# Kernel optimization log

Hardware: AMD Instinct MI355X
Metric: run time of the kernel (lower is better)

The kernel has to match this reference:

```python
import jax, jax.numpy as jnp
import numpy as np

B, R, L = 1, 256, 384
IN_DIM, PAIR_DIM, N_HEADS = 128, 128, 8
HEAD_DIM = IN_DIM // N_HEADS
FF_MULT = 4


def layer_norm(x, g, b, eps=1e-5):
    mu = jnp.mean(x, axis=-1, keepdims=True)
    var = jnp.mean((x - mu) ** 2, axis=-1, keepdims=True)
    return (x - mu) * jax.lax.rsqrt(var + eps) * g + b


def setup_inputs() -> dict:
    key = jax.random.key(0)
    ks = jax.random.split(key, 12)
    s = 0.02
    return {
        "x": jax.random.normal(ks[0], (B, L, L, PAIR_DIM), jnp.float32),
        "m": jax.random.normal(ks[1], (B, R, L, IN_DIM), jnp.float32),
        "ln1_g": jnp.ones((PAIR_DIM,), jnp.float32),
        "ln1_b": jnp.zeros((PAIR_DIM,), jnp.float32),
        "ln2_g": jnp.ones((IN_DIM,), jnp.float32),
        "ln2_b": jnp.zeros((IN_DIM,), jnp.float32),
        "ln3_g": jnp.ones((IN_DIM,), jnp.float32),
        "ln3_b": jnp.zeros((IN_DIM,), jnp.float32),
        "w1": jax.random.normal(ks[2], (PAIR_DIM, N_HEADS), jnp.float32) * s,
        "b1": jnp.zeros((N_HEADS,), jnp.float32),
        "w2": jax.random.normal(ks[3], (IN_DIM, HEAD_DIM), jnp.float32) * s,
        "b2": jnp.zeros((HEAD_DIM,), jnp.float32),
        "ffw1": jax.random.normal(ks[4], (IN_DIM, IN_DIM * FF_MULT), jnp.float32) * s,
        "ffb1": jnp.zeros((IN_DIM * FF_MULT,), jnp.float32),
        "ffw2": jax.random.normal(ks[5], (IN_DIM * FF_MULT, IN_DIM), jnp.float32) * s,
        "ffb2": jnp.zeros((IN_DIM,), jnp.float32),
    }


def reference(x, m, ln1_g, ln1_b, ln2_g, ln2_b, ln3_g, ln3_b,
              w1, b1, w2, b2, ffw1, ffb1, ffw2, ffb2):
    # symmetrize pair features: [b, i, j, d]
    pair = (x + jnp.swapaxes(x, 1, 2)) * 0.5
    pair = layer_norm(pair, ln1_g, ln1_b)
    # attention logits per head, softmax over j (axis=-2): [b, i, j, h]
    attn = jax.nn.softmax(pair @ w1 + b1, axis=-2)
    # values: [b, r, j, d_head]
    values = layer_norm(m, ln2_g, ln2_b) @ w2 + b2
    # [b,i,j,h] x [b,r,j,d] -> [b,r,i,h,d]
    attn_out = jnp.einsum('bijh,brjd->brihd', attn, values)
    attn_out = attn_out.reshape(*attn_out.shape[:3], -1)  # [b,r,i,h*d]
    out = m + attn_out
    residue = layer_norm(out, ln3_g, ln3_b)
    ff = jax.nn.relu(residue @ ffw1 + ffb1) @ ffw2 + ffb2  # dropout off (eval)
    return out + ff
```

## Files before the change

kernel.cpp:

```cpp
#include <hip/hip_runtime.h>

typedef __attribute__((ext_vector_type(8))) short bf16x8;
typedef __attribute__((ext_vector_type(4))) float f32x4;

constexpr int L  = 384;
constexpr int R  = 256;
constexpr int D  = 128;
constexpr int NH = 8;
constexpr int HD = 16;
constexpr int FF = 512;

#define MFMA16(a, b, c) __builtin_amdgcn_mfma_f32_16x16x32_bf16((a), (b), (c), 0, 0, 0)

__device__ inline unsigned short f2bf(float f) {
    unsigned u = __builtin_bit_cast(unsigned, f);
    u += 0x7fffu + ((u >> 16) & 1u);
    return (unsigned short)(u >> 16);
}
__device__ inline float bf2f(unsigned short h) {
    unsigned u = ((unsigned)h) << 16;
    return __builtin_bit_cast(float, u);
}

__device__ inline int tri_row(int q) {
    int i = (int)((769.0f - sqrtf((float)(591361 - 8 * q))) * 0.5f);
    while ((i + 1) * (769 - (i + 1)) / 2 <= q) ++i;
    while (i * (769 - i) / 2 > q) --i;
    return i;
}

__global__ void k_prep(const float* __restrict__ w1,
                       const float* __restrict__ w2,
                       const float* __restrict__ ffw1,
                       const float* __restrict__ ffw2,
                       const float* __restrict__ g3,
                       const float* __restrict__ b3,
                       const float* __restrict__ ffb1,
                       unsigned short* __restrict__ w1p,
                       unsigned short* __restrict__ w2p,
                       unsigned short* __restrict__ w1gF,
                       unsigned short* __restrict__ w2tF,
                       float2* __restrict__ c1c2) {
    const int idx = blockIdx.x * 256 + threadIdx.x;
    {
        const int fi = idx >> 9, rem = idx & 511, l = rem >> 3, e = rem & 7;
        const int lr2 = l & 15, lg2 = l >> 4;
        const int n = fi >> 2, ks = fi & 3;
        const int ch = n * 16 + lr2, k = ks * 32 + lg2 * 8 + e;
        w1gF[idx] = f2bf(g3[k] * ffw1[(size_t)k * FF + ch]);
    }
    {
        const int fi = idx >> 9, rem = idx & 511, l = rem >> 3, e = rem & 7;
        const int lr2 = l & 15, lg2 = l >> 4;
        const int n = fi >> 4, Ks = fi & 15;
        const int ch = n * 16 + lr2, k = Ks * 32 + lg2 * 8 + e;
        w2tF[idx] = f2bf(ffw2[(size_t)k * D + ch]);
    }
    if (idx < 16 * D) {
        const int n = idx >> 7, k = idx & 127;
        w1p[idx] = (n < NH) ? f2bf(w1[(size_t)k * NH + n]) : (unsigned short)0;
        w2p[idx] = f2bf(w2[(size_t)k * HD + n]);
    }
    if (blockIdx.x < 2) {
        const int n = blockIdx.x * 256 + threadIdx.x;
        float c1 = 0.f, c2 = 0.f;
        for (int k = 0; k < D; ++k) {
            const float w = ffw1[(size_t)k * FF + n];
            c1 += g3[k] * w;
            c2 += b3[k] * w;
        }
        c1c2[n] = make_float2(c1, c2 + ffb1[n]);
    }
}

__global__ void k_plv(const float* __restrict__ x,
                      const float* __restrict__ g1,
                      const float* __restrict__ bt1,
                      const unsigned short* __restrict__ w1p,
                      const float* __restrict__ b1,
                      float* __restrict__ logits,
                      const float* __restrict__ m_,
                      const float* __restrict__ g2,
                      const float* __restrict__ bt2,
                      const unsigned short* __restrict__ w2p,
                      const float* __restrict__ b2,
                      unsigned short* __restrict__ VtT) {
    __shared__ unsigned short nrm[64][136];
    __shared__ int ij[64];
    const int tid = threadIdx.x;

    if (blockIdx.x < 1155) {
        const int q0 = blockIdx.x * 64;
        {
            const int pr = tid >> 2, part = tid & 3;
            const int q = q0 + pr;
            const int i = tri_row(q);
            const int j = i + (q - i * (769 - i) / 2);
            if (part == 0) ij[pr] = (i << 16) | j;
            const float* xa = x + ((size_t)i * L + j) * D + part * 32;
            const float* xb = x + ((size_t)j * L + i) * D + part * 32;
            float v[32];
            float s = 0.f, sq = 0.f;
            #pragma unroll
            for (int q8 = 0; q8 < 8; ++q8) {
                const float4 a = ((const float4*)xa)[q8];
                const float4 b = ((const float4*)xb)[q8];
                const float t0 = 0.5f * (a.x + b.x), t1 = 0.5f * (a.y + b.y);
                const float t2 = 0.5f * (a.z + b.z), t3 = 0.5f * (a.w + b.w);
                v[q8*4+0] = t0; v[q8*4+1] = t1; v[q8*4+2] = t2; v[q8*4+3] = t3;
                s  += t0 + t1 + t2 + t3;
                sq += t0*t0 + t1*t1 + t2*t2 + t3*t3;
            }
            s  += __shfl_xor(s, 1);  s  += __shfl_xor(s, 2);
            sq += __shfl_xor(sq, 1); sq += __shfl_xor(sq, 2);
            const float mean = s * (1.0f / D);
            const float rstd = rsqrtf(sq * (1.0f / D) - mean * mean + 1e-5f);
            #pragma unroll
            for (int q8 = 0; q8 < 8; ++q8) {
                const int c = part * 32 + q8 * 4;
                ushort4 pk;
                pk.x = f2bf((v[q8*4+0] - mean) * rstd * g1[c+0] + bt1[c+0]);
                pk.y = f2bf((v[q8*4+1] - mean) * rstd * g1[c+1] + bt1[c+1]);
                pk.z = f2bf((v[q8*4+2] - mean) * rstd * g1[c+2] + bt1[c+2]);
                pk.w = f2bf((v[q8*4+3] - mean) * rstd * g1[c+3] + bt1[c+3]);
                *(ushort4*)(&nrm[pr][c]) = pk;
            }
        }
        __syncthreads();
        {
            const int wv = tid >> 6, lane = tid & 63;
            const int lr = lane & 15, lg = lane >> 4;
            f32x4 acc = {0.f, 0.f, 0.f, 0.f};
            #pragma unroll
            for (int ks = 0; ks < 4; ++ks) {
                bf16x8 a = *(const bf16x8*)(&nrm[wv * 16 + lr][ks * 32 + lg * 8]);
                bf16x8 b = *(const bf16x8*)(w1p + (size_t)lr * D + ks * 32 + lg * 8);
                acc = MFMA16(a, b, acc);
            }
            if (lr < NH) {
                #pragma unroll
                for (int r = 0; r < 4; ++r) {
                    const int pl = wv * 16 + lg * 4 + r;
                    const int pij = ij[pl];
                    const int pi = pij >> 16, pj = pij & 0xffff;
                    const float val = acc[r] + b1[lr];
                    logits[((size_t)pi * L + pj) * NH + lr] = val;
                    logits[((size_t)pj * L + pi) * NH + lr] = val;
                }
            }
        }
    } else {
        const int vb = blockIdx.x - 1155;
        const int r  = vb / 6;
        const int j0 = (vb % 6) * 64;
        {
            const int row = tid >> 2, part = tid & 3;
            const float* src = m_ + ((size_t)r * L + j0 + row) * D + part * 32;
            float v[32];
            float s = 0.f, sq = 0.f;
            #pragma unroll
            for (int q = 0; q < 8; ++q) {
                const float4 a = ((const float4*)src)[q];
                v[q*4+0] = a.x; v[q*4+1] = a.y; v[q*4+2] = a.z; v[q*4+3] = a.w;
                s  += a.x + a.y + a.z + a.w;
                sq += a.x*a.x + a.y*a.y + a.z*a.z + a.w*a.w;
            }
            s  += __shfl_xor(s, 1);  s  += __shfl_xor(s, 2);
            sq += __shfl_xor(sq, 1); sq += __shfl_xor(sq, 2);
            const float mean = s * (1.0f / D);
            const float rstd = rsqrtf(sq * (1.0f / D) - mean * mean + 1e-5f);
            #pragma unroll
            for (int q = 0; q < 8; ++q) {
                const int c = part * 32 + q * 4;
                ushort4 pk;
                pk.x = f2bf((v[q*4+0] - mean) * rstd * g2[c+0] + bt2[c+0]);
                pk.y = f2bf((v[q*4+1] - mean) * rstd * g2[c+1] + bt2[c+1]);
                pk.z = f2bf((v[q*4+2] - mean) * rstd * g2[c+2] + bt2[c+2]);
                pk.w = f2bf((v[q*4+3] - mean) * rstd * g2[c+3] + bt2[c+3]);
                *(ushort4*)(&nrm[row][c]) = pk;
            }
        }
        __syncthreads();
        {
            const int wv = tid >> 6, lane = tid & 63;
            const int lr = lane & 15, lg = lane >> 4;
            f32x4 acc = {0.f, 0.f, 0.f, 0.f};
            #pragma unroll
            for (int ks = 0; ks < 4; ++ks) {
                bf16x8 b = *(const bf16x8*)(w2p + (size_t)lr * D + ks * 32 + lg * 8);
                bf16x8 a = *(const bf16x8*)(&nrm[wv * 16 + lr][ks * 32 + lg * 8]);
                acc = MFMA16(a, b, acc);
            }
            const float bb = b2[lr];
            ushort4 pk;
            pk.x = f2bf(acc[0] + bb);
            pk.y = f2bf(acc[1] + bb);
            pk.z = f2bf(acc[2] + bb);
            pk.w = f2bf(acc[3] + bb);
            *(ushort4*)(VtT + (size_t)(r * HD + lr) * L + j0 + wv * 16 + lg * 4) = pk;
        }
    }
}

__global__ void k_softmax(const float* __restrict__ logits,
                          unsigned short* __restrict__ attnT) {
    const int wave = blockIdx.x * 4 + (threadIdx.x >> 6);
    const int lane = threadIdx.x & 63;
    const int i = wave >> 3, h = wave & 7;

    float v[6];
    float mx = -1e30f;
    #pragma unroll
    for (int t = 0; t < 6; ++t) {
        const int j = lane + t * 64;
        v[t] = logits[((size_t)i * L + j) * NH + h];
        mx = fmaxf(mx, v[t]);
    }
    #pragma unroll
    for (int msk = 32; msk; msk >>= 1) mx = fmaxf(mx, __shfl_xor(mx, msk));

    float s = 0.0f;
    #pragma unroll
    for (int t = 0; t < 6; ++t) { v[t] = __expf(v[t] - mx); s += v[t]; }
    #pragma unroll
    for (int msk = 32; msk; msk >>= 1) s += __shfl_xor(s, msk);
    const float inv = 1.0f / s;

    #pragma unroll
    for (int t = 0; t < 6; ++t) {
        const int j = lane + t * 64;
        attnT[((size_t)h * L + i) * L + j] = f2bf(v[t] * inv);
    }
}

__global__ void k_attn_out(const unsigned short* __restrict__ attnT,
                           const unsigned short* __restrict__ VtT,
                           const float* __restrict__ min_,
                           unsigned short* __restrict__ outb) {
    const int h  = blockIdx.z;
    const int i0 = blockIdx.x * 128;
    const int n0 = blockIdx.y * 128;
    const int tid = threadIdx.x, wv = tid >> 6, lane = tid & 63;
    const int lr = lane & 15, lg = lane >> 4;
    const int wio = (wv >> 1) * 64, wno = (wv & 1) * 64;
    const unsigned short* Abase = attnT + (size_t)h * L * L;

    f32x4 acc[4][4];
    #pragma unroll
    for (int a = 0; a < 4; ++a)
        #pragma unroll
        for (int b = 0; b < 4; ++b) acc[a][b] = (f32x4){0.f, 0.f, 0.f, 0.f};

    bf16x8 af[4], bf[4], afn[4], bfn[4];
    #pragma unroll
    for (int mt = 0; mt < 4; ++mt)
        af[mt] = *(const bf16x8*)(Abase + (size_t)(i0 + wio + mt * 16 + lr) * L + lg * 8);
    #pragma unroll
    for (int nt = 0; nt < 4; ++nt)
        bf[nt] = *(const bf16x8*)(VtT + (size_t)(n0 + wno + nt * 16 + lr) * L + lg * 8);

    for (int ks = 0; ks < 12; ++ks) {
        if (ks < 11) {
            const int ko = (ks + 1) * 32 + lg * 8;
            #pragma unroll
            for (int mt = 0; mt < 4; ++mt)
                afn[mt] = *(const bf16x8*)(Abase + (size_t)(i0 + wio + mt * 16 + lr) * L + ko);
            #pragma unroll
            for (int nt = 0; nt < 4; ++nt)
                bfn[nt] = *(const bf16x8*)(VtT + (size_t)(n0 + wno + nt * 16 + lr) * L + ko);
        }
        #pragma unroll
        for (int mt = 0; mt < 4; ++mt)
            #pragma unroll
            for (int nt = 0; nt < 4; ++nt)
                acc[mt][nt] = MFMA16(af[mt], bf[nt], acc[mt][nt]);
        #pragma unroll
        for (int q = 0; q < 4; ++q) { af[q] = afn[q]; bf[q] = bfn[q]; }
    }

    #pragma unroll
    for (int mt = 0; mt < 4; ++mt) {
        #pragma unroll
        for (int nt = 0; nt < 4; ++nt) {
            const int nbase = n0 + wno + nt * 16;
            const int rrow  = nbase >> 4;
            #pragma unroll
            for (int r = 0; r < 4; ++r) {
                const int i = i0 + wio + mt * 16 + lg * 4 + r;
                const size_t gidx = ((size_t)rrow * L + i) * D + h * HD + lr;
                outb[gidx] = f2bf(min_[gidx] + acc[mt][nt][r]);
            }
        }
    }
}

__global__ __launch_bounds__(512, 4) void k_ffn(
                      const unsigned short* __restrict__ outb,
                      const unsigned short* __restrict__ w1gF,
                      const float2* __restrict__ c1c2,
                      const unsigned short* __restrict__ w2tF,
                      const float* __restrict__ ffb2,
                      float* __restrict__ out) {
    __shared__ unsigned short At[64 * 128];
    __shared__ unsigned short hid[2][64 * 128];
    __shared__ float2 stats[64];
    const int tid = threadIdx.x;
    const size_t row0 = (size_t)blockIdx.x * 64;

    const int wv = tid >> 6, lane = tid & 63;
    const int lr = lane & 15, lg = lane >> 4;
    const int wm = wv >> 2, wn = wv & 3;

    bf16x8 w1f[8], w2f[8];
    #pragma unroll
    for (int ks = 0; ks < 4; ++ks)
        #pragma unroll
        for (int nt = 0; nt < 2; ++nt) {
            const int fi = (0 * 8 + wn * 2 + nt) * 4 + ks;
            w1f[ks * 2 + nt] = *(const bf16x8*)((const char*)w1gF + fi * 1024 + lane * 16);
        }

    {
        const int rr = tid >> 3, part = tid & 7;
        const unsigned short* src = outb + (row0 + rr) * D + part * 16;
        const uint4 v0 = *(const uint4*)(src);
        const uint4 v1 = *(const uint4*)(src + 8);
        float s = 0.f, sq = 0.f;
        const unsigned w[8] = {v0.x, v0.y, v0.z, v0.w, v1.x, v1.y, v1.z, v1.w};
        #pragma unroll
        for (int e = 0; e < 8; ++e) {
            const float lo = __builtin_bit_cast(float, w[e] << 16);
            const float hi = __builtin_bit_cast(float, w[e] & 0xffff0000u);
            s  += lo + hi;
            sq += lo * lo + hi * hi;
        }
        s  += __shfl_xor(s, 1);  s  += __shfl_xor(s, 2);  s  += __shfl_xor(s, 4);
        sq += __shfl_xor(sq, 1); sq += __shfl_xor(sq, 2); sq += __shfl_xor(sq, 4);
        if (part == 0) {
            const float mean = s * (1.0f / D);
            const float rstd = rsqrtf(sq * (1.0f / D) - mean * mean + 1e-5f);
            stats[rr] = make_float2(rstd, mean * rstd);
        }
        const int xr = (rr & 7) << 4;
        char* rowp = (char*)(At + rr * 128);
        const int cb = part * 32;
        *(uint4*)(rowp + ((cb     ) ^ xr)) = v0;
        *(uint4*)(rowp + ((cb + 16) ^ xr)) = v1;
    }

    #pragma unroll
    for (int ks = 0; ks < 4; ++ks)
        #pragma unroll
        for (int nt = 0; nt < 2; ++nt) {
            const int fi = (wn * 2 + nt) * 16 + 0 * 4 + ks;
            w2f[ks * 2 + nt] = *(const bf16x8*)((const char*)w2tF + fi * 1024 + lane * 16);
        }

    __syncthreads();

    f32x4 acc2[2][2];
    #pragma unroll
    for (int m = 0; m < 2; ++m)
        #pragma unroll
        for (int n = 0; n < 2; ++n) acc2[m][n] = (f32x4){0.f, 0.f, 0.f, 0.f};

    #pragma unroll
    for (int kc = 0; kc < 4; ++kc) {
        const int p = kc & 1;

        {
            f32x4 acc1[2][2];
            #pragma unroll
            for (int m = 0; m < 2; ++m)
                #pragma unroll
                for (int n = 0; n < 2; ++n) acc1[m][n] = (f32x4){0.f, 0.f, 0.f, 0.f};

            #pragma unroll
            for (int ks = 0; ks < 4; ++ks) {
                bf16x8 af[2];
                #pragma unroll
                for (int mt = 0; mt < 2; ++mt) {
                    const int row = wm * 32 + mt * 16 + lr;
                    af[mt] = *(const bf16x8*)((char*)(At + row * 128) +
                              ((ks * 64 + lg * 16) ^ ((row & 7) << 4)));
                }
                #pragma unroll
                for (int mt = 0; mt < 2; ++mt)
                    #pragma unroll
                    for (int nt = 0; nt < 2; ++nt)
                        acc1[mt][nt] = MFMA16(af[mt], w1f[ks * 2 + nt], acc1[mt][nt]);
            }

            #pragma unroll
            for (int nt = 0; nt < 2; ++nt) {
                const int chl = wn * 32 + nt * 16 + lr;
                const float2 cc = c1c2[kc * 128 + chl];
                #pragma unroll
                for (int mt = 0; mt < 2; ++mt) {
                    #pragma unroll
                    for (int r = 0; r < 4; ++r) {
                        const int row = wm * 32 + mt * 16 + lg * 4 + r;
                        const float2 st = stats[row];
                        const float pre = st.x * acc1[mt][nt][r] - st.y * cc.x + cc.y;
                        *(unsigned short*)((char*)(hid[p] + row * 128) +
                            ((chl * 2) ^ ((row & 7) << 4))) = f2bf(fmaxf(pre, 0.f));
                    }
                }
            }
        }
        __syncthreads();

        if (kc < 3) {
            #pragma unroll
            for (int ks = 0; ks < 4; ++ks)
                #pragma unroll
                for (int nt = 0; nt < 2; ++nt) {
                    const int fi = ((kc + 1) * 8 + wn * 2 + nt) * 4 + ks;
                    w1f[ks * 2 + nt] = *(const bf16x8*)((const char*)w1gF + fi * 1024 + lane * 16);
                }
        }

        {
            #pragma unroll
            for (int ks = 0; ks < 4; ++ks) {
                bf16x8 hf[2];
                #pragma unroll
                for (int mt = 0; mt < 2; ++mt) {
                    const int row = wm * 32 + mt * 16 + lr;
                    hf[mt] = *(const bf16x8*)((char*)(hid[p] + row * 128) +
                              ((ks * 64 + lg * 16) ^ ((row & 7) << 4)));
                }
                #pragma unroll
                for (int mt = 0; mt < 2; ++mt)
                    #pragma unroll
                    for (int nt = 0; nt < 2; ++nt)
                        acc2[mt][nt] = MFMA16(hf[mt], w2f[ks * 2 + nt], acc2[mt][nt]);
            }
        }

        if (kc < 3) {
            #pragma unroll
            for (int ks = 0; ks < 4; ++ks)
                #pragma unroll
                for (int nt = 0; nt < 2; ++nt) {
                    const int fi = (wn * 2 + nt) * 16 + (kc + 1) * 4 + ks;
                    w2f[ks * 2 + nt] = *(const bf16x8*)((const char*)w2tF + fi * 1024 + lane * 16);
                }
        }
    }

    #pragma unroll
    for (int nt = 0; nt < 2; ++nt) {
        const int ch = wn * 32 + nt * 16 + lr;
        const float bb = ffb2[ch];
        #pragma unroll
        for (int mt = 0; mt < 2; ++mt) {
            #pragma unroll
            for (int r = 0; r < 4; ++r) {
                const int row = wm * 32 + mt * 16 + lg * 4 + r;
                const float resid = bf2f(*(const unsigned short*)((char*)(At + row * 128) +
                                     ((ch * 2) ^ ((row & 7) << 4))));
                out[(row0 + row) * (size_t)D + ch] = resid + acc2[mt][nt][r] + bb;
            }
        }
    }
}

extern "C" void kernel_launch(void* const* d_in, const int* in_sizes, int n_in,
                              void* d_out, int out_size, void* d_ws, size_t ws_size,
                              hipStream_t stream) {
    const float* x     = (const float*)d_in[0];
    const float* m     = (const float*)d_in[1];
    const float* ln1_g = (const float*)d_in[2];
    const float* ln1_b = (const float*)d_in[3];
    const float* ln2_g = (const float*)d_in[4];
    const float* ln2_b = (const float*)d_in[5];
    const float* ln3_g = (const float*)d_in[6];
    const float* ln3_b = (const float*)d_in[7];
    const float* w1    = (const float*)d_in[8];
    const float* b1    = (const float*)d_in[9];
    const float* w2    = (const float*)d_in[10];
    const float* b2    = (const float*)d_in[11];
    const float* ffw1  = (const float*)d_in[12];
    const float* ffb1  = (const float*)d_in[13];
    const float* ffw2  = (const float*)d_in[14];
    const float* ffb2  = (const float*)d_in[15];

    float* out = (float*)d_out;

    char* wsp = (char*)d_ws;
    float*          logits = (float*)wsp;              wsp += (size_t)L*L*NH*4;
    unsigned short* attnT  = (unsigned short*)wsp;     wsp += (size_t)NH*L*L*2;
    unsigned short* VtT    = (unsigned short*)wsp;     wsp += (size_t)R*HD*L*2;
    unsigned short* w1gF   = (unsigned short*)wsp;     wsp += (size_t)FF*D*2;
    unsigned short* w2tF   = (unsigned short*)wsp;     wsp += (size_t)D*FF*2;
    unsigned short* w1p    = (unsigned short*)wsp;     wsp += (size_t)16*D*2;
    unsigned short* w2p    = (unsigned short*)wsp;     wsp += (size_t)16*D*2;
    float2*         c1c2   = (float2*)wsp;             wsp += (size_t)FF*8;
    unsigned short* outb   = (unsigned short*)wsp;     wsp += (size_t)R*L*D*2;

    k_prep<<<(FF * D) / 256, 256, 0, stream>>>(w1, w2, ffw1, ffw2,
                                               ln3_g, ln3_b, ffb1,
                                               w1p, w2p, w1gF, w2tF, c1c2);

    k_plv<<<1155 + R * 6, 256, 0, stream>>>(x, ln1_g, ln1_b, w1p, b1, logits,
                                            m, ln2_g, ln2_b, w2p, b2, VtT);

    k_softmax<<<(L * NH) / 4, 256, 0, stream>>>(logits, attnT);

    dim3 g4(L / 128, (R * HD) / 128, NH);
    k_attn_out<<<g4, 256, 0, stream>>>(attnT, VtT, m, outb);

    k_ffn<<<(R * L) / 64, 512, 0, stream>>>(outb, w1gF, c1c2, w2tF, ffb2, out);
}
```

Measured before the change: 145.1 us.

## Tile pair symmetrization into 8x8 blocks with LDS-staged transpose

The pair LayerNorm/logit stage now assigns each block an 8x8 tile pair from the upper triangle of a 48x48 tile grid, replacing a flat triangular enumeration of 64 individual pairs. The transposed tile x[j,i] is staged through a swizzled shared-memory buffer so both tiles are read as contiguous runs. The aim is better locality for the transposed reads and less per-thread index arithmetic. In exchange it adds an extra barrier and LDS traffic, and diagonal tiles redo some symmetric pairs.

```diff
diff --git a/kernel.cpp b/kernel.cpp
--- a/kernel.cpp
+++ b/kernel.cpp
@@ -10,6 +10,9 @@
 constexpr int HD = 16;
 constexpr int FF = 512;
 
+constexpr int NTILE  = 48;
+constexpr int NPAIRT = NTILE * (NTILE + 1) / 2;
+
 #define MFMA16(a, b, c) __builtin_amdgcn_mfma_f32_16x16x32_bf16((a), (b), (c), 0, 0, 0)
 
 __device__ inline unsigned short f2bf(float f) {
@@ -20,13 +23,6 @@
 __device__ inline float bf2f(unsigned short h) {
     unsigned u = ((unsigned)h) << 16;
     return __builtin_bit_cast(float, u);
-}
-
-__device__ inline int tri_row(int q) {
-    int i = (int)((769.0f - sqrtf((float)(591361 - 8 * q))) * 0.5f);
-    while ((i + 1) * (769 - (i + 1)) / 2 <= q) ++i;
-    while (i * (769 - i) / 2 > q) --i;
-    return i;
 }
 
 __global__ void k_prep(const float* __restrict__ w1,
@@ -85,57 +81,86 @@
                       const unsigned short* __restrict__ w2p,
                       const float* __restrict__ b2,
                       unsigned short* __restrict__ VtT) {
-    __shared__ unsigned short nrm[64][136];
+    __shared__ __align__(16) char smem[32768];
     __shared__ int ij[64];
+    float* xstage = (float*)smem;
+    unsigned short (*nrm)[136] = (unsigned short(*)[136])smem;
     const int tid = threadIdx.x;
 
-    if (blockIdx.x < 1155) {
-        const int q0 = blockIdx.x * 64;
-        {
-            const int pr = tid >> 2, part = tid & 3;
-            const int q = q0 + pr;
-            const int i = tri_row(q);
-            const int j = i + (q - i * (769 - i) / 2);
-            if (part == 0) ij[pr] = (i << 16) | j;
-            const float* xa = x + ((size_t)i * L + j) * D + part * 32;
-            const float* xb = x + ((size_t)j * L + i) * D + part * 32;
-            float v[32];
-            float s = 0.f, sq = 0.f;
+    if (blockIdx.x < NPAIRT) {
+        const int q = blockIdx.x;
+        int t = (int)((97.0f - sqrtf((float)(9409 - 8 * q))) * 0.5f);
+        while ((t + 1) * (97 - (t + 1)) / 2 <= q) ++t;
+        while (t * (97 - t) / 2 > q) --t;
+        const int ti = t;
+        const int tj = t + (q - t * (97 - t) / 2);
+
+        const int pr = tid >> 2, part = tid & 3;
+        const int il = pr >> 3, jl = pr & 7;
+        const int i = ti * 8 + il, j = tj * 8 + jl;
+        if (part == 0) ij[pr] = (i << 16) | j;
+
+        const float4* xa = (const float4*)(x + ((size_t)i * L + j) * D + part * 32);
+        float4 a[8];
+        #pragma unroll
+        for (int q8 = 0; q8 < 8; ++q8) a[q8] = xa[q8];
+
+        {
+            const int sw  = pr;
+            const int swz = (sw ^ (sw >> 3)) & 7;
+            const float4* xbsrc = (const float4*)(x +
+                ((size_t)(tj * 8 + il) * L + (ti * 8 + jl)) * D + part * 32);
+            float* rowp = xstage + sw * 128 + part * 32;
+            #pragma unroll
+            for (int q8 = 0; q8 < 8; ++q8)
+                *(float4*)(rowp + ((q8 ^ swz) << 2)) = xbsrc[q8];
+        }
+        __syncthreads();
+
+        float v[32];
+        float s = 0.f, sq = 0.f;
+        {
+            const int sr  = jl * 8 + il;
+            const int swz = (sr ^ (sr >> 3)) & 7;
+            const float* rowp = xstage + sr * 128 + part * 32;
             #pragma unroll
             for (int q8 = 0; q8 < 8; ++q8) {
-                const float4 a = ((const float4*)xa)[q8];
-                const float4 b = ((const float4*)xb)[q8];
-                const float t0 = 0.5f * (a.x + b.x), t1 = 0.5f * (a.y + b.y);
-                const float t2 = 0.5f * (a.z + b.z), t3 = 0.5f * (a.w + b.w);
+                const float4 b = *(const float4*)(rowp + ((q8 ^ swz) << 2));
+                const float t0 = 0.5f * (a[q8].x + b.x), t1 = 0.5f * (a[q8].y + b.y);
+                const float t2 = 0.5f * (a[q8].z + b.z), t3 = 0.5f * (a[q8].w + b.w);
                 v[q8*4+0] = t0; v[q8*4+1] = t1; v[q8*4+2] = t2; v[q8*4+3] = t3;
                 s  += t0 + t1 + t2 + t3;
                 sq += t0*t0 + t1*t1 + t2*t2 + t3*t3;
             }
-            s  += __shfl_xor(s, 1);  s  += __shfl_xor(s, 2);
-            sq += __shfl_xor(sq, 1); sq += __shfl_xor(sq, 2);
-            const float mean = s * (1.0f / D);
-            const float rstd = rsqrtf(sq * (1.0f / D) - mean * mean + 1e-5f);
-            #pragma unroll
-            for (int q8 = 0; q8 < 8; ++q8) {
-                const int c = part * 32 + q8 * 4;
-                ushort4 pk;
-                pk.x = f2bf((v[q8*4+0] - mean) * rstd * g1[c+0] + bt1[c+0]);
-                pk.y = f2bf((v[q8*4+1] - mean) * rstd * g1[c+1] + bt1[c+1]);
-                pk.z = f2bf((v[q8*4+2] - mean) * rstd * g1[c+2] + bt1[c+2]);
-                pk.w = f2bf((v[q8*4+3] - mean) * rstd * g1[c+3] + bt1[c+3]);
-                *(ushort4*)(&nrm[pr][c]) = pk;
-            }
-        }
+        }
+        s  += __shfl_xor(s, 1);  s  += __shfl_xor(s, 2);
+        sq += __shfl_xor(sq, 1); sq += __shfl_xor(sq, 2);
+        const float mean = s * (1.0f / D);
+        const float rstd = rsqrtf(sq * (1.0f / D) - mean * mean + 1e-5f);
+
         __syncthreads();
+
+        #pragma unroll
+        for (int q8 = 0; q8 < 8; ++q8) {
+            const int c = part * 32 + q8 * 4;
+            ushort4 pk;
+            pk.x = f2bf((v[q8*4+0] - mean) * rstd * g1[c+0] + bt1[c+0]);
+            pk.y = f2bf((v[q8*4+1] - mean) * rstd * g1[c+1] + bt1[c+1]);
+            pk.z = f2bf((v[q8*4+2] - mean) * rstd * g1[c+2] + bt1[c+2]);
+            pk.w = f2bf((v[q8*4+3] - mean) * rstd * g1[c+3] + bt1[c+3]);
+            *(ushort4*)(&nrm[pr][c]) = pk;
+        }
+        __syncthreads();
+
         {
             const int wv = tid >> 6, lane = tid & 63;
             const int lr = lane & 15, lg = lane >> 4;
             f32x4 acc = {0.f, 0.f, 0.f, 0.f};
             #pragma unroll
             for (int ks = 0; ks < 4; ++ks) {
-                bf16x8 a = *(const bf16x8*)(&nrm[wv * 16 + lr][ks * 32 + lg * 8]);
-                bf16x8 b = *(const bf16x8*)(w1p + (size_t)lr * D + ks * 32 + lg * 8);
-                acc = MFMA16(a, b, acc);
+                bf16x8 av = *(const bf16x8*)(&nrm[wv * 16 + lr][ks * 32 + lg * 8]);
+                bf16x8 bv = *(const bf16x8*)(w1p + (size_t)lr * D + ks * 32 + lg * 8);
+                acc = MFMA16(av, bv, acc);
             }
             if (lr < NH) {
                 #pragma unroll
@@ -150,7 +175,7 @@
             }
         }
     } else {
-        const int vb = blockIdx.x - 1155;
+        const int vb = blockIdx.x - NPAIRT;
         const int r  = vb / 6;
         const int j0 = (vb % 6) * 64;
         {
@@ -503,8 +528,8 @@
                                                ln3_g, ln3_b, ffb1,
                                                w1p, w2p, w1gF, w2tF, c1c2);
 
-    k_plv<<<1155 + R * 6, 256, 0, stream>>>(x, ln1_g, ln1_b, w1p, b1, logits,
-                                            m, ln2_g, ln2_b, w2p, b2, VtT);
+    k_plv<<<NPAIRT + R * 6, 256, 0, stream>>>(x, ln1_g, ln1_b, w1p, b1, logits,
+                                              m, ln2_g, ln2_b, w2p, b2, VtT);
 
     k_softmax<<<(L * NH) / 4, 256, 0, stream>>>(logits, attnT);
 
```

Measured after the change: 142.8 us, median of 2. Within noise of the previous version (-1.6%).
